# Performance work log

Hardware: AMD Instinct MI355X
Metric: run time of the kernel (lower is better)

The kernel has to match this reference:

```python
import jax, jax.numpy as jnp
import numpy as np

NUM_HEADS = 16
HEAD_DIM = 64  # 1024 / 16


def setup_inputs() -> dict:
    key = jax.random.key(0)
    k1, k2, k3 = jax.random.split(key, 3)
    B, S, D = 4, 1024, 1024
    hidden_states = jax.random.normal(k1, (B, S, D), dtype=jnp.float32)
    W_attn = jax.random.normal(k2, (D, 3 * D), dtype=jnp.float32) * 0.02
    b_attn = jnp.zeros((3 * D,), dtype=jnp.float32)
    W_proj = jax.random.normal(k3, (D, D), dtype=jnp.float32) * 0.02
    b_proj = jnp.zeros((D,), dtype=jnp.float32)
    return {"hidden_states": hidden_states, "W_attn": W_attn, "b_attn": b_attn,
            "W_proj": W_proj, "b_proj": b_proj}


def reference(hidden_states, W_attn, b_attn, W_proj, b_proj):
    B, S, D = hidden_states.shape
    H, Hd = NUM_HEADS, HEAD_DIM
    # fused QKV projection (Conv1D: x @ W + b)
    qkv = hidden_states @ W_attn + b_attn  # [B,S,3D]
    q, k, v = jnp.split(qkv, 3, axis=-1)
    # [B,H,S,Hd]
    q = q.reshape(B, S, H, Hd).transpose(0, 2, 1, 3)
    k = k.reshape(B, S, H, Hd).transpose(0, 2, 1, 3)
    v = v.reshape(B, S, H, Hd).transpose(0, 2, 1, 3)
    # scores [B,H,S,S], scaled by sqrt(head_dim)
    scores = jnp.einsum('bhqd,bhkd->bhqk', q, k) / jnp.asarray(
        Hd ** 0.5, dtype=q.dtype)
    # causal mask (torch.where(causal, scores, finfo.min))
    causal = jnp.tril(jnp.ones((S, S), dtype=bool))
    mask_value = jnp.finfo(scores.dtype).min
    scores = jnp.where(causal[None, None], scores, mask_value)
    attn_weights = jax.nn.softmax(scores, axis=-1)
    # dropout p=0 (eval) -> identity
    attn_output = jnp.einsum('bhqk,bhkd->bhqd', attn_weights, v)  # [B,H,S,Hd]
    attn_output = attn_output.transpose(0, 2, 1, 3).reshape(B, S, D)
    attn_output = attn_output @ W_proj + b_proj
    return attn_output, attn_weights
```

## Files before the change

kernel.cpp:

```cpp
#include <hip/hip_runtime.h>

typedef __attribute__((ext_vector_type(8))) short bf16x8;
typedef __attribute__((ext_vector_type(4))) short short4v;
typedef __attribute__((ext_vector_type(4))) float f32x4;

__device__ __forceinline__ short f2bf(float f) {
  union { float f; unsigned u; } v; v.f = f;
  unsigned u = v.u;
  u += 0x7fffu + ((u >> 16) & 1u);
  return (short)(u >> 16);
}
__device__ __forceinline__ float bf2f(short s) {
  union { unsigned u; float f; } v;
  v.u = ((unsigned)(unsigned short)s) << 16;
  return v.f;
}

__device__ __forceinline__ void gl_lds16(const short* g, short* l) {
  __builtin_amdgcn_global_load_lds(
      (const __attribute__((address_space(1))) unsigned int*)g,
      (__attribute__((address_space(3))) unsigned int*)l, 16, 0, 0);
}

__global__ void cvt_bf16(const float* __restrict__ src, short* __restrict__ dst, int n) {
  int i = (blockIdx.x * 256 + threadIdx.x) * 4;
  if (i >= n) return;
  f32x4 v = *(const f32x4*)(src + i);
  short4v o;
  o.x = f2bf(v.x); o.y = f2bf(v.y); o.z = f2bf(v.z); o.w = f2bf(v.w);
  *(short4v*)(dst + i) = o;
}

__global__ void transpose_cvt(const float* __restrict__ src, short* __restrict__ dst,
                              int K, int N) {
  __shared__ float t[32][33];
  int n0 = blockIdx.x * 32, k0 = blockIdx.y * 32;
  int c = threadIdx.x & 31, r8 = threadIdx.x >> 5;
#pragma unroll
  for (int p = 0; p < 4; ++p) {
    int r = r8 + p * 8;
    t[r][c] = src[(k0 + r) * (long)N + n0 + c];
  }
  __syncthreads();
#pragma unroll
  for (int p = 0; p < 4; ++p) {
    int r = r8 + p * 8;
    dst[(n0 + r) * (long)K + k0 + c] = f2bf(t[c][r]);
  }
}

__global__ __launch_bounds__(256) void gemm_qkv(
    const short* __restrict__ A, const short* __restrict__ BT,
    const float* __restrict__ bias,
    short* __restrict__ Qo, short* __restrict__ Ko, short* __restrict__ Vo,
    int M, int N, int K) {
  __shared__ short As[128 * 32];
  __shared__ short Bs[128 * 32];
  int tid = threadIdx.x;
  int wave = tid >> 6, lane = tid & 63;
  int quad = lane >> 4, l16 = lane & 15;
  int lin = blockIdx.y * gridDim.x + blockIdx.x;
  int nbk = gridDim.y;
  int mg = lin >> 3;
  int m0 = ((lin & 7) + (mg / nbk) * 8) * 128;
  int n0 = (mg % nbk) * 128;
  int wr = wave >> 1, wc = wave & 1;

  f32x4 zero = {0.f, 0.f, 0.f, 0.f};
  f32x4 acc[4][4];
#pragma unroll
  for (int i = 0; i < 4; ++i)
#pragma unroll
    for (int j = 0; j < 4; ++j) acc[i][j] = zero;

  int r0 = tid >> 2, c8 = (tid & 3) * 8;
  int wbase = (tid & 192) * 8;

  for (int kt = 0; kt < K; kt += 32) {
    const short* Ab = A + (long)m0 * K + kt;
    const short* Bb = BT + (long)n0 * K + kt;
#pragma unroll
    for (int c = 0; c < 2; ++c) {
      gl_lds16(Ab + (long)(c * 64 + r0) * K + c8, &As[c * 2048 + wbase]);
      gl_lds16(Bb + (long)(c * 64 + r0) * K + c8, &Bs[c * 2048 + wbase]);
    }
    __syncthreads();
    bf16x8 af[4], bfv[4];
#pragma unroll
    for (int i = 0; i < 4; ++i)
      af[i] = *(const bf16x8*)(&As[(wr * 64 + i * 16 + l16) * 32 + quad * 8]);
#pragma unroll
    for (int j = 0; j < 4; ++j)
      bfv[j] = *(const bf16x8*)(&Bs[(wc * 64 + j * 16 + l16) * 32 + quad * 8]);
#pragma unroll
    for (int i = 0; i < 4; ++i)
#pragma unroll
      for (int j = 0; j < 4; ++j)
        acc[i][j] = __builtin_amdgcn_mfma_f32_16x16x32_bf16(af[i], bfv[j], acc[i][j], 0, 0, 0);
    __syncthreads();
  }

#pragma unroll
  for (int i = 0; i < 4; ++i) {
    int m_base = m0 + wr * 64 + i * 16 + quad * 4;
#pragma unroll
    for (int j = 0; j < 4; ++j) {
      int n = n0 + wc * 64 + j * 16 + l16;
      float bv = bias[n];
      int region = n >> 10;
      int nn = n & 1023;
      int h = nn >> 6, d = nn & 63;
      int b = m_base >> 10, s = m_base & 1023;
      if (region == 2) {
        short4v pk;
#pragma unroll
        for (int r = 0; r < 4; ++r) pk[r] = f2bf(acc[i][j][r] + bv);
        *(short4v*)(&Vo[((b * 16 + h) * 64 + d) * 1024 + s]) = pk;
      } else {
        short* dst = (region == 0) ? Qo : Ko;
#pragma unroll
        for (int r = 0; r < 4; ++r)
          dst[((b * 16 + h) * 1024 + (s + r)) * 64 + d] = f2bf(acc[i][j][r] + bv);
      }
    }
  }
}

__global__ __launch_bounds__(256) void gemm_proj(
    const short* __restrict__ A, const short* __restrict__ BT,
    const float* __restrict__ bias, float* __restrict__ Cout,
    int M, int N, int K) {
  __shared__ short As[128 * 32];
  __shared__ short Bs[64 * 32];
  int tid = threadIdx.x;
  int wave = tid >> 6, lane = tid & 63;
  int quad = lane >> 4, l16 = lane & 15;
  int m0 = blockIdx.x * 128, n0 = blockIdx.y * 64;

  f32x4 zero = {0.f, 0.f, 0.f, 0.f};
  f32x4 acc[2][4];
#pragma unroll
  for (int i = 0; i < 2; ++i)
#pragma unroll
    for (int j = 0; j < 4; ++j) acc[i][j] = zero;

  int r0 = tid >> 2, c8 = (tid & 3) * 8;
  int wbase = (tid & 192) * 8;

  for (int kt = 0; kt < K; kt += 32) {
    const short* Ab = A + (long)m0 * K + kt;
    const short* Bb = BT + (long)n0 * K + kt;
#pragma unroll
    for (int c = 0; c < 2; ++c)
      gl_lds16(Ab + (long)(c * 64 + r0) * K + c8, &As[c * 2048 + wbase]);
    gl_lds16(Bb + (long)r0 * K + c8, &Bs[wbase]);
    __syncthreads();
    bf16x8 af[2], bfv[4];
#pragma unroll
    for (int i = 0; i < 2; ++i)
      af[i] = *(const bf16x8*)(&As[(wave * 32 + i * 16 + l16) * 32 + quad * 8]);
#pragma unroll
    for (int j = 0; j < 4; ++j)
      bfv[j] = *(const bf16x8*)(&Bs[(j * 16 + l16) * 32 + quad * 8]);
#pragma unroll
    for (int i = 0; i < 2; ++i)
#pragma unroll
      for (int j = 0; j < 4; ++j)
        acc[i][j] = __builtin_amdgcn_mfma_f32_16x16x32_bf16(af[i], bfv[j], acc[i][j], 0, 0, 0);
    __syncthreads();
  }

#pragma unroll
  for (int i = 0; i < 2; ++i) {
    int m_base = m0 + wave * 32 + i * 16 + quad * 4;
#pragma unroll
    for (int j = 0; j < 4; ++j) {
      int n = n0 + j * 16 + l16;
      float bv = bias[n];
#pragma unroll
      for (int r = 0; r < 4; ++r)
        Cout[(long)(m_base + r) * N + n] = acc[i][j][r] + bv;
    }
  }
}

#define SWZ(m, k) ((m) * 1024 + ((((k) >> 3) ^ ((m) & 7)) << 3) + ((k) & 7))

__global__ __launch_bounds__(256) void attn_fused(
    const short* __restrict__ Q, const short* __restrict__ Km,
    const short* __restrict__ Vt, float* __restrict__ Wout,
    short* __restrict__ Oout) {
  __shared__ short sc[16 * 1024];
  __shared__ float s_part[4][16];
  __shared__ float s_inv[16];
  int tid = threadIdx.x;
  int wave = tid >> 6, lane = tid & 63;
  int quad = lane >> 4, l16 = lane & 15;
  int qt = blockIdx.x;
  int bh = blockIdx.y;
  int q0 = qt * 16;
  const short* Qb = Q + (long)bh * 65536;
  const short* Kb = Km + (long)bh * 65536;
  const short* Vb = Vt + (long)bh * 65536;

  bf16x8 aq0 = *(const bf16x8*)(Qb + (q0 + l16) * 64 + quad * 8);
  bf16x8 aq1 = *(const bf16x8*)(Qb + (q0 + l16) * 64 + 32 + quad * 8);
  f32x4 zero = {0.f, 0.f, 0.f, 0.f};
  float rs[4] = {0.f, 0.f, 0.f, 0.f};
  for (int t = wave; t <= qt; t += 4) {
    int ks0 = t * 16;
    bf16x8 bk0 = *(const bf16x8*)(Kb + (ks0 + l16) * 64 + quad * 8);
    bf16x8 bk1 = *(const bf16x8*)(Kb + (ks0 + l16) * 64 + 32 + quad * 8);
    f32x4 d = zero;
    d = __builtin_amdgcn_mfma_f32_16x16x32_bf16(aq0, bk0, d, 0, 0, 0);
    d = __builtin_amdgcn_mfma_f32_16x16x32_bf16(aq1, bk1, d, 0, 0, 0);
#pragma unroll
    for (int r = 0; r < 4; ++r) {
      float e;
      if (t == qt && l16 > quad * 4 + r) e = 0.f;
      else e = __expf(d[r] * 0.125f);
      rs[r] += e;
      sc[SWZ(quad * 4 + r, ks0 + l16)] = f2bf(e);
    }
  }
  if (!(qt & 1) && wave == ((qt + 1) & 3)) {
#pragma unroll
    for (int r = 0; r < 4; ++r)
      sc[SWZ(quad * 4 + r, (qt + 1) * 16 + l16)] = 0;
  }
#pragma unroll
  for (int r = 0; r < 4; ++r) {
#pragma unroll
    for (int o = 1; o < 16; o <<= 1) rs[r] += __shfl_xor(rs[r], o, 64);
  }
  if (l16 == 0) {
#pragma unroll
    for (int r = 0; r < 4; ++r) s_part[wave][quad * 4 + r] = rs[r];
  }
  __syncthreads();
  if (tid < 16)
    s_inv[tid] = 1.f / (s_part[0][tid] + s_part[1][tid] + s_part[2][tid] + s_part[3][tid]);
  __syncthreads();

  {
    int m = wave * 4 + quad;
    int qg = q0 + m;
    float inv = s_inv[m];
    float* wrow = Wout + ((long)bh * 1024 + qg) * 1024;
#pragma unroll
    for (int ib = 0; ib < 8; ++ib) {
      int kbase = (ib * 16 + l16) * 8;
      f32x4 w0 = zero, w1 = zero;
      if (kbase <= qg) {
        bf16x8 e = *(const bf16x8*)(&sc[SWZ(m, kbase)]);
#pragma unroll
        for (int j = 0; j < 4; ++j) w0[j] = bf2f(e[j]) * inv;
#pragma unroll
        for (int j = 0; j < 4; ++j) w1[j] = bf2f(e[j + 4]) * inv;
      }
      __builtin_nontemporal_store(w0, (f32x4*)(wrow + kbase));
      __builtin_nontemporal_store(w1, (f32x4*)(wrow + kbase + 4));
    }
  }

  int d0 = wave * 16;
  f32x4 o0 = zero, o1 = zero;
  int nsteps = (q0 + 47) >> 5;
  int s = 0;
  for (; s + 2 <= nsteps; s += 2) {
    int ksA = s * 32, ksB = s * 32 + 32;
    bf16x8 afA = *(const bf16x8*)(&sc[l16 * 1024 + ((((ksA >> 3) + quad) ^ (l16 & 7)) << 3)]);
    bf16x8 bvA = *(const bf16x8*)(Vb + (d0 + l16) * 1024 + ksA + quad * 8);
    bf16x8 afB = *(const bf16x8*)(&sc[l16 * 1024 + ((((ksB >> 3) + quad) ^ (l16 & 7)) << 3)]);
    bf16x8 bvB = *(const bf16x8*)(Vb + (d0 + l16) * 1024 + ksB + quad * 8);
    o0 = __builtin_amdgcn_mfma_f32_16x16x32_bf16(afA, bvA, o0, 0, 0, 0);
    o1 = __builtin_amdgcn_mfma_f32_16x16x32_bf16(afB, bvB, o1, 0, 0, 0);
  }
  if (s < nsteps) {
    int ks0 = s * 32;
    bf16x8 af = *(const bf16x8*)(&sc[l16 * 1024 + ((((ks0 >> 3) + quad) ^ (l16 & 7)) << 3)]);
    bf16x8 bv = *(const bf16x8*)(Vb + (d0 + l16) * 1024 + ks0 + quad * 8);
    o0 = __builtin_amdgcn_mfma_f32_16x16x32_bf16(af, bv, o0, 0, 0, 0);
  }
  int b = bh >> 4, h = bh & 15;
#pragma unroll
  for (int r = 0; r < 4; ++r) {
    int mm = quad * 4 + r;
    float val = (o0[r] + o1[r]) * s_inv[mm];
    Oout[((long)b * 1024 + (q0 + mm)) * 1024 + h * 64 + d0 + l16] = f2bf(val);
  }
}

extern "C" void kernel_launch(void* const* d_in, const int* in_sizes, int n_in,
                              void* d_out, int out_size, void* d_ws, size_t ws_size,
                              hipStream_t stream) {
  const float* hidden = (const float*)d_in[0];
  const float* W_attn = (const float*)d_in[1];
  const float* b_attn = (const float*)d_in[2];
  const float* W_proj = (const float*)d_in[3];
  const float* b_proj = (const float*)d_in[4];

  float* out_attn = (float*)d_out;
  float* out_w = (float*)d_out + 4194304;

  char* ws = (char*)d_ws;
  short* hid_bf = (short*)(ws);
  short* wattn_t = (short*)(ws + (8u << 20));
  short* wproj_t = (short*)(ws + (14u << 20));
  short* Qb = (short*)(ws + (16u << 20));
  short* Kb = (short*)(ws + (24u << 20));
  short* Vt = (short*)(ws + (32u << 20));
  short* Ao = (short*)(ws + (40u << 20));

  cvt_bf16<<<4096, 256, 0, stream>>>(hidden, hid_bf, 4096 * 1024);
  transpose_cvt<<<dim3(96, 32), 256, 0, stream>>>(W_attn, wattn_t, 1024, 3072);
  transpose_cvt<<<dim3(32, 32), 256, 0, stream>>>(W_proj, wproj_t, 1024, 1024);

  gemm_qkv<<<dim3(32, 24), 256, 0, stream>>>(hid_bf, wattn_t, b_attn,
                                             Qb, Kb, Vt, 4096, 3072, 1024);

  attn_fused<<<dim3(64, 64), 256, 0, stream>>>(Qb, Kb, Vt, out_w, Ao);

  gemm_proj<<<dim3(32, 16), 256, 0, stream>>>(Ao, wproj_t, b_proj, out_attn,
                                              4096, 1024, 1024);
}
```

Baseline: 440.7 us.

## Merge prep kernels, double K-step per barrier in GEMMs, coalesce weight stores

Replaces the three conversion/transpose launches with a single prep kernel that dispatches on block index, removing two launches. Both GEMMs now load two 32-wide K slices per iteration into split LDS buffers, halving the number of barrier pairs per K loop at the cost of doubled LDS use. The attention-weights writeback is restructured so each wave writes one full contiguous row segment per store (lane*4 floats), making the global stores fully coalesced instead of strided 8-float chunks per lane.

```diff
diff --git a/kernel.cpp b/kernel.cpp
--- a/kernel.cpp
+++ b/kernel.cpp
@@ -22,20 +22,26 @@
       (__attribute__((address_space(3))) unsigned int*)l, 16, 0, 0);
 }
 
-__global__ void cvt_bf16(const float* __restrict__ src, short* __restrict__ dst, int n) {
-  int i = (blockIdx.x * 256 + threadIdx.x) * 4;
-  if (i >= n) return;
-  f32x4 v = *(const f32x4*)(src + i);
-  short4v o;
-  o.x = f2bf(v.x); o.y = f2bf(v.y); o.z = f2bf(v.z); o.w = f2bf(v.w);
-  *(short4v*)(dst + i) = o;
-}
-
-__global__ void transpose_cvt(const float* __restrict__ src, short* __restrict__ dst,
-                              int K, int N) {
+__global__ void prep(const float* __restrict__ hidden, short* __restrict__ hid_bf,
+                     const float* __restrict__ W_attn, short* __restrict__ wattn_t,
+                     const float* __restrict__ W_proj, short* __restrict__ wproj_t) {
   __shared__ float t[32][33];
-  int n0 = blockIdx.x * 32, k0 = blockIdx.y * 32;
-  int c = threadIdx.x & 31, r8 = threadIdx.x >> 5;
+  int b = blockIdx.x, tid = threadIdx.x;
+  if (b < 4096) {
+    int i = (b * 256 + tid) * 4;
+    f32x4 v = *(const f32x4*)(hidden + i);
+    short4v o;
+    o.x = f2bf(v.x); o.y = f2bf(v.y); o.z = f2bf(v.z); o.w = f2bf(v.w);
+    *(short4v*)(hid_bf + i) = o;
+    return;
+  }
+  const float* src; short* dst; int N, bb;
+  if (b < 7168) { bb = b - 4096; N = 3072; src = W_attn; dst = wattn_t; }
+  else          { bb = b - 7168; N = 1024; src = W_proj; dst = wproj_t; }
+  const int K = 1024;
+  int nx = N >> 5;
+  int n0 = (bb % nx) * 32, k0 = (bb / nx) * 32;
+  int c = tid & 31, r8 = tid >> 5;
 #pragma unroll
   for (int p = 0; p < 4; ++p) {
     int r = r8 + p * 8;
@@ -54,8 +60,8 @@
     const float* __restrict__ bias,
     short* __restrict__ Qo, short* __restrict__ Ko, short* __restrict__ Vo,
     int M, int N, int K) {
-  __shared__ short As[128 * 32];
-  __shared__ short Bs[128 * 32];
+  __shared__ short As[2][4096];
+  __shared__ short Bs[2][4096];
   int tid = threadIdx.x;
   int wave = tid >> 6, lane = tid & 63;
   int quad = lane >> 4, l16 = lane & 15;
@@ -76,27 +82,33 @@
   int r0 = tid >> 2, c8 = (tid & 3) * 8;
   int wbase = (tid & 192) * 8;
 
-  for (int kt = 0; kt < K; kt += 32) {
+  for (int kt = 0; kt < K; kt += 64) {
     const short* Ab = A + (long)m0 * K + kt;
     const short* Bb = BT + (long)n0 * K + kt;
 #pragma unroll
-    for (int c = 0; c < 2; ++c) {
-      gl_lds16(Ab + (long)(c * 64 + r0) * K + c8, &As[c * 2048 + wbase]);
-      gl_lds16(Bb + (long)(c * 64 + r0) * K + c8, &Bs[c * 2048 + wbase]);
+    for (int h = 0; h < 2; ++h) {
+#pragma unroll
+      for (int c = 0; c < 2; ++c) {
+        gl_lds16(Ab + (long)(c * 64 + r0) * K + h * 32 + c8, &As[h][c * 2048 + wbase]);
+        gl_lds16(Bb + (long)(c * 64 + r0) * K + h * 32 + c8, &Bs[h][c * 2048 + wbase]);
+      }
     }
     __syncthreads();
-    bf16x8 af[4], bfv[4];
-#pragma unroll
-    for (int i = 0; i < 4; ++i)
-      af[i] = *(const bf16x8*)(&As[(wr * 64 + i * 16 + l16) * 32 + quad * 8]);
-#pragma unroll
-    for (int j = 0; j < 4; ++j)
-      bfv[j] = *(const bf16x8*)(&Bs[(wc * 64 + j * 16 + l16) * 32 + quad * 8]);
-#pragma unroll
-    for (int i = 0; i < 4; ++i)
+#pragma unroll
+    for (int h = 0; h < 2; ++h) {
+      bf16x8 af[4], bfv[4];
+#pragma unroll
+      for (int i = 0; i < 4; ++i)
+        af[i] = *(const bf16x8*)(&As[h][(wr * 64 + i * 16 + l16) * 32 + quad * 8]);
 #pragma unroll
       for (int j = 0; j < 4; ++j)
-        acc[i][j] = __builtin_amdgcn_mfma_f32_16x16x32_bf16(af[i], bfv[j], acc[i][j], 0, 0, 0);
+        bfv[j] = *(const bf16x8*)(&Bs[h][(wc * 64 + j * 16 + l16) * 32 + quad * 8]);
+#pragma unroll
+      for (int i = 0; i < 4; ++i)
+#pragma unroll
+        for (int j = 0; j < 4; ++j)
+          acc[i][j] = __builtin_amdgcn_mfma_f32_16x16x32_bf16(af[i], bfv[j], acc[i][j], 0, 0, 0);
+    }
     __syncthreads();
   }
 
@@ -130,8 +142,8 @@
     const short* __restrict__ A, const short* __restrict__ BT,
     const float* __restrict__ bias, float* __restrict__ Cout,
     int M, int N, int K) {
-  __shared__ short As[128 * 32];
-  __shared__ short Bs[64 * 32];
+  __shared__ short As[2][4096];
+  __shared__ short Bs[2][2048];
   int tid = threadIdx.x;
   int wave = tid >> 6, lane = tid & 63;
   int quad = lane >> 4, l16 = lane & 15;
@@ -147,26 +159,32 @@
   int r0 = tid >> 2, c8 = (tid & 3) * 8;
   int wbase = (tid & 192) * 8;
 
-  for (int kt = 0; kt < K; kt += 32) {
+  for (int kt = 0; kt < K; kt += 64) {
     const short* Ab = A + (long)m0 * K + kt;
     const short* Bb = BT + (long)n0 * K + kt;
 #pragma unroll
-    for (int c = 0; c < 2; ++c)
-      gl_lds16(Ab + (long)(c * 64 + r0) * K + c8, &As[c * 2048 + wbase]);
-    gl_lds16(Bb + (long)r0 * K + c8, &Bs[wbase]);
+    for (int h = 0; h < 2; ++h) {
+#pragma unroll
+      for (int c = 0; c < 2; ++c)
+        gl_lds16(Ab + (long)(c * 64 + r0) * K + h * 32 + c8, &As[h][c * 2048 + wbase]);
+      gl_lds16(Bb + (long)r0 * K + h * 32 + c8, &Bs[h][wbase]);
+    }
     __syncthreads();
-    bf16x8 af[2], bfv[4];
-#pragma unroll
-    for (int i = 0; i < 2; ++i)
-      af[i] = *(const bf16x8*)(&As[(wave * 32 + i * 16 + l16) * 32 + quad * 8]);
-#pragma unroll
-    for (int j = 0; j < 4; ++j)
-      bfv[j] = *(const bf16x8*)(&Bs[(j * 16 + l16) * 32 + quad * 8]);
-#pragma unroll
-    for (int i = 0; i < 2; ++i)
+#pragma unroll
+    for (int h = 0; h < 2; ++h) {
+      bf16x8 af[2], bfv[4];
+#pragma unroll
+      for (int i = 0; i < 2; ++i)
+        af[i] = *(const bf16x8*)(&As[h][(wave * 32 + i * 16 + l16) * 32 + quad * 8]);
 #pragma unroll
       for (int j = 0; j < 4; ++j)
-        acc[i][j] = __builtin_amdgcn_mfma_f32_16x16x32_bf16(af[i], bfv[j], acc[i][j], 0, 0, 0);
+        bfv[j] = *(const bf16x8*)(&Bs[h][(j * 16 + l16) * 32 + quad * 8]);
+#pragma unroll
+      for (int i = 0; i < 2; ++i)
+#pragma unroll
+        for (int j = 0; j < 4; ++j)
+          acc[i][j] = __builtin_amdgcn_mfma_f32_16x16x32_bf16(af[i], bfv[j], acc[i][j], 0, 0, 0);
+    }
     __syncthreads();
   }
 
@@ -242,24 +260,25 @@
     s_inv[tid] = 1.f / (s_part[0][tid] + s_part[1][tid] + s_part[2][tid] + s_part[3][tid]);
   __syncthreads();
 
-  {
-    int m = wave * 4 + quad;
+#pragma unroll
+  for (int r = 0; r < 4; ++r) {
+    int m = wave * 4 + r;
     int qg = q0 + m;
     float inv = s_inv[m];
     float* wrow = Wout + ((long)bh * 1024 + qg) * 1024;
 #pragma unroll
-    for (int ib = 0; ib < 8; ++ib) {
-      int kbase = (ib * 16 + l16) * 8;
-      f32x4 w0 = zero, w1 = zero;
-      if (kbase <= qg) {
-        bf16x8 e = *(const bf16x8*)(&sc[SWZ(m, kbase)]);
-#pragma unroll
-        for (int j = 0; j < 4; ++j) w0[j] = bf2f(e[j]) * inv;
-#pragma unroll
-        for (int j = 0; j < 4; ++j) w1[j] = bf2f(e[j + 4]) * inv;
+    for (int s = 0; s < 4; ++s) {
+      int col8 = s * 256 + (lane & 62) * 4;
+      f32x4 w = zero;
+      if (col8 <= qg) {
+        bf16x8 e = *(const bf16x8*)(&sc[SWZ(m, col8)]);
+        int j0 = (lane & 1) * 4;
+        w[0] = bf2f(e[j0]) * inv;
+        w[1] = bf2f(e[j0 + 1]) * inv;
+        w[2] = bf2f(e[j0 + 2]) * inv;
+        w[3] = bf2f(e[j0 + 3]) * inv;
       }
-      __builtin_nontemporal_store(w0, (f32x4*)(wrow + kbase));
-      __builtin_nontemporal_store(w1, (f32x4*)(wrow + kbase + 4));
+      __builtin_nontemporal_store(w, (f32x4*)(wrow + s * 256 + lane * 4));
     }
   }
 
@@ -312,9 +331,7 @@
   short* Vt = (short*)(ws + (32u << 20));
   short* Ao = (short*)(ws + (40u << 20));
 
-  cvt_bf16<<<4096, 256, 0, stream>>>(hidden, hid_bf, 4096 * 1024);
-  transpose_cvt<<<dim3(96, 32), 256, 0, stream>>>(W_attn, wattn_t, 1024, 3072);
-  transpose_cvt<<<dim3(32, 32), 256, 0, stream>>>(W_proj, wproj_t, 1024, 1024);
+  prep<<<8192, 256, 0, stream>>>(hidden, hid_bf, W_attn, wattn_t, W_proj, wproj_t);
 
   gemm_qkv<<<dim3(32, 24), 256, 0, stream>>>(hid_bf, wattn_t, b_attn,
                                              Qb, Kb, Vt, 4096, 3072, 1024);
```

New measurement: 425.7 us. 3.4% less time.
